# Kernel tuning notes

Hardware: AMD Instinct MI355X
Metric: run time of the kernel (lower is better)

The kernel has to match this reference:

```python
import jax, jax.numpy as jnp
import numpy as np


def _gather_neighbours(h, idx):
    # h: (B, N, H); idx: (B, N, K) int -> (B, N, K, H)
    B, N, H = h.shape
    K = idx.shape[-1]
    flat = idx.reshape(B, N * K)  # (B, N*K)
    rep = jnp.take_along_axis(h, flat[..., None], axis=1)  # (B, N*K, H)
    return rep.reshape(B, N, K, H)


def _masked_agg(h, idx, mask):
    # gather neighbor hidden states then masked sum over neighbors -> (B, N, H)
    rep = _gather_neighbours(h, idx)
    return jnp.einsum('bnkh,bnk->bnh', rep, mask)


def setup_inputs() -> dict:
    key = jax.random.key(0)
    ks = jax.random.split(key, 12)
    B, N, H, K = 8, 2000, 128, 32
    s = 1.0 / np.sqrt(H)
    return {
        'node_hidden': jax.random.normal(ks[0], (B, N, H), jnp.float32),
        'cell': jax.random.normal(ks[1], (B, N, H), jnp.float32),
        'w_in': jax.random.normal(ks[2], (4, H, H), jnp.float32) * s,
        'w_out': jax.random.normal(ks[3], (4, H, H), jnp.float32) * s,
        'u_in': jax.random.normal(ks[4], (4, H, H), jnp.float32) * s,
        'u_out': jax.random.normal(ks[5], (4, H, H), jnp.float32) * s,
        'b': jax.random.normal(ks[6], (4, H), jnp.float32) * 0.1,
        'in_node_mask': jax.random.uniform(ks[7], (B, N, K), jnp.float32),
        'out_node_mask': jax.random.uniform(ks[8], (B, N, K), jnp.float32),
        'in_node_index': jax.random.randint(ks[9], (B, N, K), 0, N, jnp.int32),
        'out_node_index': jax.random.randint(ks[10], (B, N, K), 0, N, jnp.int32),
        'layer_num': 2,
    }


def reference(node_hidden, cell, w_in, w_out, u_in, u_out, b,
              in_node_mask, out_node_mask, in_node_index, out_node_index,
              layer_num):
    h, c = node_hidden, cell
    for _ in range(layer_num):
        in_agg = _masked_agg(h, in_node_index, in_node_mask)    # (B,N,H)
        out_agg = _masked_agg(h, out_node_index, out_node_mask)  # (B,N,H)
        # gate pre-activations, gate order: i, o, f, cell
        pre = (jnp.einsum('bnh,ghd->gbnd', in_agg, w_in)
               + jnp.einsum('bnh,ghd->gbnd', out_agg, w_out)
               + jnp.einsum('bnh,ghd->gbnd', h, u_in)
               + jnp.einsum('bnh,ghd->gbnd', h, u_out)
               + b[:, None, None, :])
        i_g = jax.nn.sigmoid(pre[0])
        o_g = jax.nn.sigmoid(pre[1])
        f_g = jax.nn.sigmoid(pre[2])
        g = jnp.tanh(pre[3])
        c = f_g * c + i_g * g
        h = o_g * jnp.tanh(c)
    return h
```

## Files before the change

### kernel.cpp

```cpp
#include <hip/hip_runtime.h>
#include <math.h>

#define B_ 8
#define N_ 2000
#define H_ 128
#define K_ 32
#define M_ (B_*N_)
#define KTOT 384
#define NC 512
#define NTILES 32
#define NCHUNK 12

typedef __attribute__((ext_vector_type(8))) short s8_t;
typedef __attribute__((ext_vector_type(4))) float f4_t;

__device__ __forceinline__ unsigned short f2bf(float x) {
    union { float f; unsigned u; } v; v.f = x;
    unsigned r = v.u + 0x7fff + ((v.u >> 16) & 1);
    return (unsigned short)(r >> 16);
}
__device__ __forceinline__ float bf2f(unsigned short b) {
    union { unsigned u; float f; } v; v.u = (unsigned)b << 16; return v.f;
}
__device__ __forceinline__ float sigm_(float x) { return 1.f / (1.f + __expf(-x)); }
__device__ __forceinline__ float tanh_(float x) { return 2.f / (1.f + __expf(-2.f * x)) - 1.f; }

__device__ __forceinline__ float pickv(f4_t A, int m) {
    float ab = (m & 1) ? A.y : A.x;
    float cd = (m & 1) ? A.w : A.z;
    return (m & 2) ? cd : ab;
}
__device__ __forceinline__ float pick4(float u0, float u1, float u2, float u3, int m) {
    float ab = (m & 1) ? u1 : u0;
    float cd = (m & 1) ? u3 : u2;
    return (m & 2) ? cd : ab;
}

__device__ __forceinline__ void split4(const float* f, ushort4& hi, ushort4& lo) {
    unsigned short h0 = f2bf(f[0]), h1 = f2bf(f[1]), h2 = f2bf(f[2]), h3 = f2bf(f[3]);
    hi = make_ushort4(h0, h1, h2, h3);
    lo = make_ushort4(f2bf(f[0] - bf2f(h0)), f2bf(f[1] - bf2f(h1)),
                      f2bf(f[2] - bf2f(h2)), f2bf(f[3] - bf2f(h3)));
}

__global__ __launch_bounds__(512)
void prep_kernel(const float* __restrict__ w_in,
                 const float* __restrict__ w_out,
                 const float* __restrict__ u_in,
                 const float* __restrict__ u_out,
                 unsigned short* __restrict__ wp_hi,
                 unsigned short* __restrict__ wp_lo) {
    int blk = blockIdx.x;
    int ntile = blk / NCHUNK, chunk = blk % NCHUNK;
    int t = threadIdx.x;
    int lane = t >> 3, e = t & 7;
    int col = ntile * 16 + (lane & 15);
    int k = chunk * 32 + (lane >> 4) * 8 + e;
    int d = col >> 2, g = col & 3;
    float v;
    if (k < 128) {
        v = w_in[(g * 128 + k) * 128 + d];
    } else if (k < 256) {
        v = w_out[(g * 128 + (k - 128)) * 128 + d];
    } else {
        int kk = k - 256;
        v = u_in[(g * 128 + kk) * 128 + d] + u_out[(g * 128 + kk) * 128 + d];
    }
    unsigned short hs = f2bf(v);
    wp_hi[(size_t)blk * 512 + t] = hs;
    wp_lo[(size_t)blk * 512 + t] = f2bf(v - bf2f(hs));
}

__global__ __launch_bounds__(256)
void agg_kernel(const float* __restrict__ h,
                const int* __restrict__ in_idx,
                const float* __restrict__ in_mask,
                const int* __restrict__ out_idx,
                const float* __restrict__ out_mask,
                unsigned short* __restrict__ A_hi,
                unsigned short* __restrict__ A_lo) {
    int bid = (blockIdx.x & 7) * 250 + (blockIdx.x >> 3);
    int tid = threadIdx.x;
    int r = tid >> 5;
    int p = tid & 31;
    int row = bid * 8 + r;
    int b = row / N_;
    const float* hb = h + (size_t)b * N_ * H_;

    __shared__ int   s_idx[8][64];
    __shared__ float s_msk[8][64];
    for (int e = tid; e < 512; e += 256) {
        int r2 = e >> 6, q = e & 63;
        int ridx = bid * 8 + r2;
        if (q < 32) {
            s_idx[r2][q] = in_idx[ridx * K_ + q];
            s_msk[r2][q] = in_mask[ridx * K_ + q];
        } else {
            s_idx[r2][q] = out_idx[ridx * K_ + (q - 32)];
            s_msk[r2][q] = out_mask[ridx * K_ + (q - 32)];
        }
    }
    __syncthreads();

    int d0 = p * 4;
    float ai[4] = {0.f, 0.f, 0.f, 0.f};
    float ao[4] = {0.f, 0.f, 0.f, 0.f};
    #pragma unroll 4
    for (int k = 0; k < K_; ++k) {
        int   i1 = s_idx[r][k];
        float m1 = s_msk[r][k];
        int   i2 = s_idx[r][32 + k];
        float m2 = s_msk[r][32 + k];
        float4 v1 = *(const float4*)(hb + (size_t)i1 * H_ + d0);
        float4 v2 = *(const float4*)(hb + (size_t)i2 * H_ + d0);
        ai[0] += m1 * v1.x; ai[1] += m1 * v1.y; ai[2] += m1 * v1.z; ai[3] += m1 * v1.w;
        ao[0] += m2 * v2.x; ao[1] += m2 * v2.y; ao[2] += m2 * v2.z; ao[3] += m2 * v2.w;
    }
    float4 hv4 = *(const float4*)(h + (size_t)row * H_ + d0);
    float hh[4] = {hv4.x, hv4.y, hv4.z, hv4.w};

    int mtile = row >> 4;
    int kg = (p >> 1) & 3;
    int e0 = (p & 1) * 4;
    int lane = (row & 15) + 16 * kg;
    size_t bi = ((size_t)(mtile * NCHUNK +     (p >> 3)) * 64 + lane) * 8 + e0;
    size_t bo = ((size_t)(mtile * NCHUNK + 4 + (p >> 3)) * 64 + lane) * 8 + e0;
    size_t bh = ((size_t)(mtile * NCHUNK + 8 + (p >> 3)) * 64 + lane) * 8 + e0;

    ushort4 hi, lo;
    split4(ai, hi, lo); *(ushort4*)(A_hi + bi) = hi; *(ushort4*)(A_lo + bi) = lo;
    split4(ao, hi, lo); *(ushort4*)(A_hi + bo) = hi; *(ushort4*)(A_lo + bo) = lo;
    split4(hh, hi, lo); *(ushort4*)(A_hi + bh) = hi; *(ushort4*)(A_lo + bh) = lo;
}

__global__ __launch_bounds__(256)
void gemm_gates(const unsigned short* __restrict__ A_hi,
                const unsigned short* __restrict__ A_lo,
                const unsigned short* __restrict__ wp_hi,
                const unsigned short* __restrict__ wp_lo,
                const float* __restrict__ bias,
                const float* __restrict__ c_src,
                float* __restrict__ c_dst,
                float* __restrict__ h_dst,
                int write_c) {
    int tid  = threadIdx.x;
    int mt   = blockIdx.x;
    int jt   = blockIdx.y;
    int lane = tid & 63;
    int w    = tid >> 6;
    int row0 = mt * 64;
    int m_off = (w & 1) * 32;
    int n_off = (w >> 1) * 64;

    int mtile0 = mt * 4 + (w & 1) * 2;
    int ntile0 = jt * 8 + (w >> 1) * 4;

    const unsigned short* pa0 = A_hi + ((size_t)mtile0 * NCHUNK * 64 + lane) * 8;
    const unsigned short* pa1 = A_lo + ((size_t)mtile0 * NCHUNK * 64 + lane) * 8;
    const unsigned short* pb0 = wp_hi + ((size_t)ntile0 * NCHUNK * 64 + lane) * 8;
    const unsigned short* pb1 = wp_lo + ((size_t)ntile0 * NCHUNK * 64 + lane) * 8;
    const size_t mstride = (size_t)NCHUNK * 512;
    const size_t cstride = 512;

    f4_t zero = {0.f, 0.f, 0.f, 0.f};
    f4_t acc[2][4];
    #pragma unroll
    for (int i = 0; i < 2; ++i)
        #pragma unroll
        for (int j = 0; j < 4; ++j) acc[i][j] = zero;

    s8_t ahA[2], alA[2], bhA[4], blA[4];
    s8_t ahB[2], alB[2], bhB[4], blB[4];

#define LOADF(ah, al, bh, bl, c)                                              \
    {                                                                         \
        _Pragma("unroll")                                                     \
        for (int i = 0; i < 2; ++i) {                                         \
            ah[i] = *(const s8_t*)(pa0 + i * mstride + (c) * cstride);        \
            al[i] = *(const s8_t*)(pa1 + i * mstride + (c) * cstride);        \
        }                                                                     \
        _Pragma("unroll")                                                     \
        for (int j = 0; j < 4; ++j) {                                         \
            bh[j] = *(const s8_t*)(pb0 + j * mstride + (c) * cstride);        \
            bl[j] = *(const s8_t*)(pb1 + j * mstride + (c) * cstride);        \
        }                                                                     \
    }

#define MFMAF(ah, al, bh, bl)                                                 \
    {                                                                         \
        _Pragma("unroll")                                                     \
        for (int i = 0; i < 2; ++i)                                           \
            _Pragma("unroll")                                                 \
            for (int j = 0; j < 4; ++j) {                                     \
                acc[i][j] = __builtin_amdgcn_mfma_f32_16x16x32_bf16(ah[i], bh[j], acc[i][j], 0, 0, 0); \
                acc[i][j] = __builtin_amdgcn_mfma_f32_16x16x32_bf16(ah[i], bl[j], acc[i][j], 0, 0, 0); \
                acc[i][j] = __builtin_amdgcn_mfma_f32_16x16x32_bf16(al[i], bh[j], acc[i][j], 0, 0, 0); \
            }                                                                 \
    }

    LOADF(ahA, alA, bhA, blA, 0)
    #pragma unroll
    for (int c = 0; c < NCHUNK; c += 2) {
        LOADF(ahB, alB, bhB, blB, c + 1)
        MFMAF(ahA, alA, bhA, blA)
        if (c + 2 < NCHUNK) LOADF(ahA, alA, bhA, blA, c + 2)
        MFMAF(ahB, alB, bhB, blB)
    }
#undef LOADF
#undef MFMAF

    int g    = lane & 3;
    int qrow = lane >> 4;
    int dl   = (lane >> 2) & 3;
    #pragma unroll
    for (int j = 0; j < 4; ++j) {
        int ncol_base = jt * 128 + n_off + j * 16;
        int d = (ncol_base >> 2) + dl;
        float b0 = bias[0 * 128 + d];
        float b1 = bias[1 * 128 + d];
        float b2 = bias[2 * 128 + d];
        float b3 = bias[3 * 128 + d];
        #pragma unroll
        for (int i = 0; i < 2; ++i) {
            f4_t A = acc[i][j];
            float s0 = pickv(A, g);
            float s1 = pickv(A, g ^ 1);
            float s2 = pickv(A, g ^ 2);
            float s3 = pickv(A, g ^ 3);
            float u0 = s0;
            float u1 = __shfl_xor(s1, 1);
            float u2 = __shfl_xor(s2, 2);
            float u3 = __shfl_xor(s3, 3);
            float p0 = pick4(u0, u1, u2, u3, g) + b0;
            float p1 = pick4(u0, u1, u2, u3, g ^ 1) + b1;
            float p2 = pick4(u0, u1, u2, u3, g ^ 2) + b2;
            float p3 = pick4(u0, u1, u2, u3, g ^ 3) + b3;
            float ig = sigm_(p0);
            float og = sigm_(p1);
            float fg = sigm_(p2);
            float cg = tanh_(p3);
            int row = row0 + m_off + i * 16 + qrow * 4 + g;
            size_t off = (size_t)row * H_ + d;
            float c_old = c_src[off];
            float c_new = fg * c_old + ig * cg;
            if (write_c) c_dst[off] = c_new;
            h_dst[off] = og * tanh_(c_new);
        }
    }
}

extern "C" void kernel_launch(void* const* d_in, const int* in_sizes, int n_in,
                              void* d_out, int out_size, void* d_ws, size_t ws_size,
                              hipStream_t stream) {
    const float* node_hidden = (const float*)d_in[0];
    const float* cell        = (const float*)d_in[1];
    const float* w_in        = (const float*)d_in[2];
    const float* w_out       = (const float*)d_in[3];
    const float* u_in        = (const float*)d_in[4];
    const float* u_out       = (const float*)d_in[5];
    const float* bias        = (const float*)d_in[6];
    const float* in_mask     = (const float*)d_in[7];
    const float* out_mask    = (const float*)d_in[8];
    const int*   in_idx      = (const int*)d_in[9];
    const int*   out_idx     = (const int*)d_in[10];
    float* out = (float*)d_out;

    char* p = (char*)d_ws;
    unsigned short* wp_hi = (unsigned short*)p; p += (size_t)NTILES * NCHUNK * 512 * 2;
    unsigned short* wp_lo = (unsigned short*)p; p += (size_t)NTILES * NCHUNK * 512 * 2;
    unsigned short* A_hi  = (unsigned short*)p; p += (size_t)(M_/16) * NCHUNK * 512 * 2;
    unsigned short* A_lo  = (unsigned short*)p; p += (size_t)(M_/16) * NCHUNK * 512 * 2;
    float* h_buf = (float*)p;                   p += (size_t)M_ * H_ * 4;

    prep_kernel<<<NTILES * NCHUNK, 512, 0, stream>>>(w_in, w_out, u_in, u_out, wp_hi, wp_lo);

    agg_kernel<<<M_ / 8, 256, 0, stream>>>(node_hidden, in_idx, in_mask,
                                           out_idx, out_mask, A_hi, A_lo);
    gemm_gates<<<dim3(M_ / 64, 4), 256, 0, stream>>>(
        A_hi, A_lo, wp_hi, wp_lo, bias, cell, out, h_buf, 1);

    agg_kernel<<<M_ / 8, 256, 0, stream>>>(h_buf, in_idx, in_mask,
                                           out_idx, out_mask, A_hi, A_lo);
    gemm_gates<<<dim3(M_ / 64, 4), 256, 0, stream>>>(
        A_hi, A_lo, wp_hi, wp_lo, bias, out, out, out, 0);
}
```

Before: 207.2 us.

## Stage GEMM operands through LDS with direct global-to-LDS loads and 128-row tiles

The gate GEMM now copies each K-chunk of the A and W hi/lo fragments into shared memory with global_load_lds, then reads them back per wave. Each block covers 128 rows instead of 64, so every wave holds a 4x4 accumulator grid and fragments are shared across waves rather than each wave loading from global memory separately. The aim is to cut redundant global/L2 traffic, but the single-buffered loop puts two barriers in every chunk and no longer overlaps loads with MFMAs. The aggregation gather loop's unroll factor also goes from 4 to 8.

```diff
diff --git a/kernel.cpp b/kernel.cpp
--- a/kernel.cpp
+++ b/kernel.cpp
@@ -41,6 +41,12 @@
     hi = make_ushort4(h0, h1, h2, h3);
     lo = make_ushort4(f2bf(f[0] - bf2f(h0)), f2bf(f[1] - bf2f(h1)),
                       f2bf(f[2] - bf2f(h2)), f2bf(f[3] - bf2f(h3)));
+}
+
+__device__ __forceinline__ void gload_lds(const unsigned short* g, short* l) {
+    __builtin_amdgcn_global_load_lds(
+        (const __attribute__((address_space(1))) unsigned*)g,
+        (__attribute__((address_space(3))) unsigned*)l, 16, 0, 0);
 }
 
 __global__ __launch_bounds__(512)
@@ -105,7 +111,7 @@
     int d0 = p * 4;
     float ai[4] = {0.f, 0.f, 0.f, 0.f};
     float ao[4] = {0.f, 0.f, 0.f, 0.f};
-    #pragma unroll 4
+    #pragma unroll 8
     for (int k = 0; k < K_; ++k) {
         int   i1 = s_idx[r][k];
         float m1 = s_msk[r][k];
@@ -143,85 +149,82 @@
                 float* __restrict__ c_dst,
                 float* __restrict__ h_dst,
                 int write_c) {
+    __shared__ short sL[32 * 512];
     int tid  = threadIdx.x;
     int mt   = blockIdx.x;
     int jt   = blockIdx.y;
     int lane = tid & 63;
     int w    = tid >> 6;
-    int row0 = mt * 64;
-    int m_off = (w & 1) * 32;
-    int n_off = (w >> 1) * 64;
-
-    int mtile0 = mt * 4 + (w & 1) * 2;
-    int ntile0 = jt * 8 + (w >> 1) * 4;
-
-    const unsigned short* pa0 = A_hi + ((size_t)mtile0 * NCHUNK * 64 + lane) * 8;
-    const unsigned short* pa1 = A_lo + ((size_t)mtile0 * NCHUNK * 64 + lane) * 8;
-    const unsigned short* pb0 = wp_hi + ((size_t)ntile0 * NCHUNK * 64 + lane) * 8;
-    const unsigned short* pb1 = wp_lo + ((size_t)ntile0 * NCHUNK * 64 + lane) * 8;
-    const size_t mstride = (size_t)NCHUNK * 512;
-    const size_t cstride = 512;
+    int wm   = w & 1;
+    int wn   = w >> 1;
+    int mtile0 = mt * 8;
+    int ntile0 = jt * 8;
+
+    const unsigned short* gp[8];
+    short* lp[8];
+    #pragma unroll
+    for (int i = 0; i < 8; ++i) {
+        int s = i * 4 + w;
+        const unsigned short* src;
+        if (s < 8)       src = A_hi  + ((size_t)((mtile0 + s)      * NCHUNK) * 64 + lane) * 8;
+        else if (s < 16) src = A_lo  + ((size_t)((mtile0 + s - 8)  * NCHUNK) * 64 + lane) * 8;
+        else if (s < 24) src = wp_hi + ((size_t)((ntile0 + s - 16) * NCHUNK) * 64 + lane) * 8;
+        else             src = wp_lo + ((size_t)((ntile0 + s - 24) * NCHUNK) * 64 + lane) * 8;
+        gp[i] = src;
+        lp[i] = &sL[s * 512];
+    }
 
     f4_t zero = {0.f, 0.f, 0.f, 0.f};
-    f4_t acc[2][4];
+    f4_t acc[4][4];
     #pragma unroll
-    for (int i = 0; i < 2; ++i)
+    for (int i = 0; i < 4; ++i)
         #pragma unroll
         for (int j = 0; j < 4; ++j) acc[i][j] = zero;
 
-    s8_t ahA[2], alA[2], bhA[4], blA[4];
-    s8_t ahB[2], alB[2], bhB[4], blB[4];
-
-#define LOADF(ah, al, bh, bl, c)                                              \
-    {                                                                         \
-        _Pragma("unroll")                                                     \
-        for (int i = 0; i < 2; ++i) {                                         \
-            ah[i] = *(const s8_t*)(pa0 + i * mstride + (c) * cstride);        \
-            al[i] = *(const s8_t*)(pa1 + i * mstride + (c) * cstride);        \
-        }                                                                     \
-        _Pragma("unroll")                                                     \
-        for (int j = 0; j < 4; ++j) {                                         \
-            bh[j] = *(const s8_t*)(pb0 + j * mstride + (c) * cstride);        \
-            bl[j] = *(const s8_t*)(pb1 + j * mstride + (c) * cstride);        \
-        }                                                                     \
-    }
-
-#define MFMAF(ah, al, bh, bl)                                                 \
-    {                                                                         \
-        _Pragma("unroll")                                                     \
-        for (int i = 0; i < 2; ++i)                                           \
-            _Pragma("unroll")                                                 \
-            for (int j = 0; j < 4; ++j) {                                     \
-                acc[i][j] = __builtin_amdgcn_mfma_f32_16x16x32_bf16(ah[i], bh[j], acc[i][j], 0, 0, 0); \
-                acc[i][j] = __builtin_amdgcn_mfma_f32_16x16x32_bf16(ah[i], bl[j], acc[i][j], 0, 0, 0); \
-                acc[i][j] = __builtin_amdgcn_mfma_f32_16x16x32_bf16(al[i], bh[j], acc[i][j], 0, 0, 0); \
-            }                                                                 \
-    }
-
-    LOADF(ahA, alA, bhA, blA, 0)
-    #pragma unroll
-    for (int c = 0; c < NCHUNK; c += 2) {
-        LOADF(ahB, alB, bhB, blB, c + 1)
-        MFMAF(ahA, alA, bhA, blA)
-        if (c + 2 < NCHUNK) LOADF(ahA, alA, bhA, blA, c + 2)
-        MFMAF(ahB, alB, bhB, blB)
-    }
-#undef LOADF
-#undef MFMAF
+    #pragma unroll 1
+    for (int c = 0; c < NCHUNK; ++c) {
+        if (c > 0) __syncthreads();
+        #pragma unroll
+        for (int i = 0; i < 8; ++i) {
+            gload_lds(gp[i], lp[i]);
+            gp[i] += 512;
+        }
+        __syncthreads();
+
+        s8_t a_hi[4], a_lo[4], b_hi[4], b_lo[4];
+        #pragma unroll
+        for (int i = 0; i < 4; ++i) {
+            a_hi[i] = *(const s8_t*)&sL[(wm * 4 + i) * 512 + lane * 8];
+            a_lo[i] = *(const s8_t*)&sL[(8 + wm * 4 + i) * 512 + lane * 8];
+        }
+        #pragma unroll
+        for (int j = 0; j < 4; ++j) {
+            b_hi[j] = *(const s8_t*)&sL[(16 + wn * 4 + j) * 512 + lane * 8];
+            b_lo[j] = *(const s8_t*)&sL[(24 + wn * 4 + j) * 512 + lane * 8];
+        }
+        #pragma unroll
+        for (int i = 0; i < 4; ++i)
+            #pragma unroll
+            for (int j = 0; j < 4; ++j) {
+                acc[i][j] = __builtin_amdgcn_mfma_f32_16x16x32_bf16(a_hi[i], b_hi[j], acc[i][j], 0, 0, 0);
+                acc[i][j] = __builtin_amdgcn_mfma_f32_16x16x32_bf16(a_hi[i], b_lo[j], acc[i][j], 0, 0, 0);
+                acc[i][j] = __builtin_amdgcn_mfma_f32_16x16x32_bf16(a_lo[i], b_hi[j], acc[i][j], 0, 0, 0);
+            }
+    }
 
     int g    = lane & 3;
     int qrow = lane >> 4;
     int dl   = (lane >> 2) & 3;
     #pragma unroll
     for (int j = 0; j < 4; ++j) {
-        int ncol_base = jt * 128 + n_off + j * 16;
+        int ncol_base = jt * 128 + wn * 64 + j * 16;
         int d = (ncol_base >> 2) + dl;
         float b0 = bias[0 * 128 + d];
         float b1 = bias[1 * 128 + d];
         float b2 = bias[2 * 128 + d];
         float b3 = bias[3 * 128 + d];
         #pragma unroll
-        for (int i = 0; i < 2; ++i) {
+        for (int i = 0; i < 4; ++i) {
             f4_t A = acc[i][j];
             float s0 = pickv(A, g);
             float s1 = pickv(A, g ^ 1);
@@ -239,7 +242,7 @@
             float og = sigm_(p1);
             float fg = sigm_(p2);
             float cg = tanh_(p3);
-            int row = row0 + m_off + i * 16 + qrow * 4 + g;
+            int row = mt * 128 + wm * 64 + i * 16 + qrow * 4 + g;
             size_t off = (size_t)row * H_ + d;
             float c_old = c_src[off];
             float c_new = fg * c_old + ig * cg;
@@ -276,11 +279,11 @@
 
     agg_kernel<<<M_ / 8, 256, 0, stream>>>(node_hidden, in_idx, in_mask,
                                            out_idx, out_mask, A_hi, A_lo);
-    gemm_gates<<<dim3(M_ / 64, 4), 256, 0, stream>>>(
+    gemm_gates<<<dim3(M_ / 128, 4), 256, 0, stream>>>(
         A_hi, A_lo, wp_hi, wp_lo, bias, cell, out, h_buf, 1);
 
     agg_kernel<<<M_ / 8, 256, 0, stream>>>(h_buf, in_idx, in_mask,
                                            out_idx, out_mask, A_hi, A_lo);
-    gemm_gates<<<dim3(M_ / 64, 4), 256, 0, stream>>>(
+    gemm_gates<<<dim3(M_ / 128, 4), 256, 0, stream>>>(
         A_hi, A_lo, wp_hi, wp_lo, bias, out, out, out, 0);
 }
```

After: 191.7 us. 7.4% less time.
